# Optimization experiments

Hardware: AMD Instinct MI355X
Metric: run time of the kernel (lower is better)

Reference implementation:

```python
import jax, jax.numpy as jnp
import numpy as np

K = 32
TEMPERATURE = 1.0
EPS = 1e-12


def setup_inputs() -> dict:
    key = jax.random.key(0)
    k1, k2, k3, k4, k5 = jax.random.split(key, 5)
    N, F, B, H, C = 65536, 512, 2048, 256, 64
    X = jax.random.normal(k1, (N, F), dtype=jnp.float32)
    # non-negative PPR-like weights (dense representation of the sparse matrix)
    ppr_scores = jax.random.uniform(k2, (B, N), dtype=jnp.float32)
    s1 = 1.0 / np.sqrt(F)
    s2 = 1.0 / np.sqrt(H)
    W1 = jax.random.uniform(k3, (F, H), dtype=jnp.float32, minval=-s1, maxval=s1)
    W2 = jax.random.uniform(k4, (H, H), dtype=jnp.float32, minval=-s2, maxval=s2)
    W3 = jax.random.uniform(k5, (H, C), dtype=jnp.float32, minval=-s2, maxval=s2)
    return {"X": X, "ppr_scores": ppr_scores, "W1": W1, "W2": W2, "W3": W3}


def _mlp(X, W1, W2, W3):
    # PPRGoMLP, nlayers=3, no bias, dropout inactive at inference
    h = jnp.maximum(X @ W1, 0.0)
    h = jnp.maximum(h @ W2, 0.0)
    return h @ W3  # [N, C] logits


def _soft_k_medoid(A, x, k=K, temperature=TEMPERATURE, with_weight_correction=True):
    # A: [B, N] ppr weights, x: [N, C] embeddings
    topk_vals, topk_idx = jax.lax.top_k(A, k)          # [B, k]
    xk = x[topk_idx]                                    # [B, k, C] gathered neighbor embeddings
    # pairwise L2 distances among the top-k neighbors of each row: [B, k, k]
    d2 = jnp.sum(jnp.square(xk[:, :, None, :] - xk[:, None, :, :]), axis=-1)
    l2 = jnp.sqrt(d2 + EPS)
    # weighted sum of distances per candidate: [B, k]
    distances = jnp.einsum('bm,bcm->bc', topk_vals, l2)
    distances = jnp.where(topk_vals == 0, jnp.finfo(distances.dtype).max, distances)
    row_sum = jnp.sum(A, axis=-1, keepdims=True)        # [B, 1]
    w = jax.nn.softmax(-distances / temperature, axis=-1)
    if with_weight_correction:
        w = w * topk_vals
        w = w / jnp.sum(w, axis=-1, keepdims=True)
    return row_sum * jnp.einsum('bk,bkc->bc', w, xk)    # [B, C]


def reference(X, ppr_scores, W1, W2, W3):
    logits = _mlp(X, W1, W2, W3)
    return _soft_k_medoid(ppr_scores, logits)
```

## Files before the change

kernel.cpp:

```cpp
#include <hip/hip_runtime.h>
#include <hip/hip_bf16.h>

typedef unsigned short u16;
typedef __attribute__((ext_vector_type(8))) __bf16 bf16x8;
typedef __attribute__((ext_vector_type(4))) float f32x4;

#define AS1 __attribute__((address_space(1)))
#define AS3 __attribute__((address_space(3)))

__device__ inline void gload_lds16(const void* g, void* l) {
  __builtin_amdgcn_global_load_lds((const AS1 void*)g, (AS3 void*)l, 16, 0, 0);
}

__device__ inline u16 f2bf(float f) {
  __bf16 h = (__bf16)f;
  return __builtin_bit_cast(u16, h);
}

__device__ inline f32x4 ldnt(const f32x4* p) {
  return __builtin_nontemporal_load(p);
}

__global__ void conv_weights(const float* __restrict__ W1, const float* __restrict__ W2,
                             const float* __restrict__ W3, u16* __restrict__ w1t,
                             u16* __restrict__ w2t, u16* __restrict__ w3t) {
  int e = blockIdx.x * 256 + threadIdx.x;
  if (e < 131072) {
    int h = e >> 9, f = e & 511;
    w1t[e] = f2bf(W1[f * 256 + h]);
  } else if (e < 196608) {
    int x = e - 131072;
    int n = x >> 8, k = x & 255;
    w2t[x] = f2bf(W2[k * 256 + n]);
  } else if (e < 212992) {
    int x = e - 196608;
    int n = x >> 8, k = x & 255;
    w3t[x] = f2bf(W3[k * 64 + n]);
  }
}

__global__ __launch_bounds__(256, 2) void mlp_kernel(const float* __restrict__ X,
                                                     const u16* __restrict__ W1t,
                                                     const u16* __restrict__ W2t,
                                                     const u16* __restrict__ W3t,
                                                     float* __restrict__ lg) {
  __shared__ alignas(16) char smem[73728];
  u16* As   = (u16*)smem;
  u16* Bs   = (u16*)(smem + 8192);
  u16* h1s  = (u16*)(smem + 40960);
  u16* quad = (u16*)smem;
  u16* w3s  = (u16*)(smem + 8192);
  const int bm = blockIdx.x, t = threadIdx.x;
  const int wid = t >> 6, lane = t & 63;
  const int wr = wid >> 1, wc = wid & 1;
  const int l15 = lane & 15, lk = lane >> 4;
  const f32x4 z = {0.f, 0.f, 0.f, 0.f};

  {
    f32x4 acc[2][8];
#pragma unroll
    for (int i = 0; i < 2; ++i)
#pragma unroll
      for (int j = 0; j < 8; ++j) acc[i][j] = z;

    for (int k0 = 0; k0 < 512; k0 += 64) {
#pragma unroll
      for (int it = 0; it < 8; ++it) {
        int s = it * 256 + t;
        int n = s >> 3;
        int koff = ((s ^ (n & 7)) & 7) * 8;
        gload_lds16(W1t + (size_t)n * 512 + k0 + koff, &Bs[s * 8]);
      }
#pragma unroll
      for (int it = 0; it < 2; ++it) {
        int s = it * 256 + t;
        int row = s >> 3, c = s & 7;
        const float* src = X + (size_t)(bm * 64 + row) * 512 + k0 + c * 8;
        float4 v0 = *(const float4*)src;
        float4 v1 = *(const float4*)(src + 4);
        bf16x8 wv;
        wv[0] = (__bf16)v0.x; wv[1] = (__bf16)v0.y; wv[2] = (__bf16)v0.z; wv[3] = (__bf16)v0.w;
        wv[4] = (__bf16)v1.x; wv[5] = (__bf16)v1.y; wv[6] = (__bf16)v1.z; wv[7] = (__bf16)v1.w;
        *(bf16x8*)&As[(row * 64 + c * 8) ^ ((row & 7) << 3)] = wv;
      }
      __syncthreads();
#pragma unroll
      for (int ks = 0; ks < 2; ++ks) {
        bf16x8 af[2], bfr[8];
#pragma unroll
        for (int i = 0; i < 2; ++i) {
          int row = wr * 32 + i * 16 + l15;
          af[i] = *(const bf16x8*)&As[(row * 64 + ks * 32 + lk * 8) ^ ((row & 7) << 3)];
        }
#pragma unroll
        for (int j = 0; j < 8; ++j) {
          int n = wc * 128 + j * 16 + l15;
          bfr[j] = *(const bf16x8*)&Bs[(n * 64 + ks * 32 + lk * 8) ^ ((n & 7) << 3)];
        }
#pragma unroll
        for (int i = 0; i < 2; ++i)
#pragma unroll
          for (int j = 0; j < 8; ++j)
            acc[i][j] = __builtin_amdgcn_mfma_f32_16x16x32_bf16(af[i], bfr[j], acc[i][j], 0, 0, 0);
      }
      __syncthreads();
    }
#pragma unroll
    for (int i = 0; i < 2; ++i)
#pragma unroll
      for (int j = 0; j < 8; ++j)
#pragma unroll
        for (int r = 0; r < 4; ++r) {
          int row = wr * 32 + i * 16 + lk * 4 + r;
          int col = wc * 128 + j * 16 + l15;
          h1s[(row * 256 + col) ^ ((row & 7) << 3)] = f2bf(fmaxf(acc[i][j][r], 0.f));
        }
    __syncthreads();
  }

  f32x4 acc2[2][8];
#pragma unroll
  for (int i = 0; i < 2; ++i)
#pragma unroll
    for (int j = 0; j < 8; ++j) acc2[i][j] = z;

  for (int k0 = 0; k0 < 256; k0 += 64) {
#pragma unroll
    for (int it = 0; it < 8; ++it) {
      int s = it * 256 + t;
      int n = s >> 3;
      int koff = ((s ^ (n & 7)) & 7) * 8;
      gload_lds16(W2t + (size_t)n * 256 + k0 + koff, &Bs[s * 8]);
    }
    __syncthreads();
#pragma unroll
    for (int ks = 0; ks < 2; ++ks) {
      bf16x8 af[2], bfr[8];
#pragma unroll
      for (int i = 0; i < 2; ++i) {
        int row = wr * 32 + i * 16 + l15;
        af[i] = *(const bf16x8*)&h1s[(row * 256 + k0 + ks * 32 + lk * 8) ^ ((row & 7) << 3)];
      }
#pragma unroll
      for (int j = 0; j < 8; ++j) {
        int n = wc * 128 + j * 16 + l15;
        bfr[j] = *(const bf16x8*)&Bs[(n * 64 + ks * 32 + lk * 8) ^ ((n & 7) << 3)];
      }
#pragma unroll
      for (int i = 0; i < 2; ++i)
#pragma unroll
        for (int j = 0; j < 8; ++j)
          acc2[i][j] = __builtin_amdgcn_mfma_f32_16x16x32_bf16(af[i], bfr[j], acc2[i][j], 0, 0, 0);
    }
    __syncthreads();
  }

  f32x4 acc3[4];
#pragma unroll
  for (int j = 0; j < 4; ++j) acc3[j] = z;

#pragma unroll
  for (int kk = 0; kk < 4; ++kk) {
    if (wc == (kk >> 1)) {
#pragma unroll
      for (int i = 0; i < 2; ++i)
#pragma unroll
        for (int j4 = 0; j4 < 4; ++j4) {
          int j = (kk & 1) * 4 + j4;
#pragma unroll
          for (int r = 0; r < 4; ++r) {
            int row = wr * 32 + i * 16 + lk * 4 + r;
            int c   = j4 * 16 + l15;
            quad[(row * 64 + c) ^ ((row & 7) << 3)] = f2bf(fmaxf(acc2[i][j][r], 0.f));
          }
        }
    }
#pragma unroll
    for (int it = 0; it < 2; ++it) {
      int s = it * 256 + t;
      int col = s >> 3;
      int koff = ((s ^ (col & 7)) & 7) * 8;
      gload_lds16(W3t + (size_t)col * 256 + kk * 64 + koff, &w3s[(it * 256 + wid * 64) * 8]);
    }
    __syncthreads();
    bf16x8 af2, bfr2[4];
#pragma unroll
    for (int ks = 0; ks < 2; ++ks) {
#pragma unroll
      for (int j2 = 0; j2 < 4; ++j2) {
        int col = j2 * 16 + l15;
        bfr2[j2] = *(const bf16x8*)&w3s[(col * 64 + ks * 32 + lk * 8) ^ ((col & 7) << 3)];
      }
      {
        int row = wid * 16 + l15;
        af2 = *(const bf16x8*)&quad[(row * 64 + ks * 32 + lk * 8) ^ ((row & 7) << 3)];
      }
#pragma unroll
      for (int j2 = 0; j2 < 4; ++j2)
        acc3[j2] = __builtin_amdgcn_mfma_f32_16x16x32_bf16(af2, bfr2[j2], acc3[j2], 0, 0, 0);
    }
    __syncthreads();
  }

#pragma unroll
  for (int j2 = 0; j2 < 4; ++j2) {
    int col = j2 * 16 + l15;
#pragma unroll
    for (int r = 0; r < 4; ++r) {
      int row = wid * 16 + lk * 4 + r;
      lg[(size_t)(bm * 64 + row) * 64 + col] = acc3[j2][r];
    }
  }
}

__global__ __launch_bounds__(256) void topk_medoid(const float* __restrict__ ppr,
                                                   const float* __restrict__ lg,
                                                   float* __restrict__ out) {
  __shared__ alignas(16) char smem[13312];
  float* cvals   = (float*)smem;
  int*   cidx    = (int*)(smem + 4096);
  float* xk      = (float*)smem;
  float* l2m     = (float*)(smem + 8448);
  float* vals    = (float*)(smem + 12672);
  int*   idxs    = (int*)(smem + 12800);
  float* dist    = (float*)(smem + 12928);
  float* wgt     = (float*)(smem + 13056);
  float* partial = (float*)(smem + 13184);
  int*   cnt     = (int*)(smem + 13200);
  float* rsum    = (float*)(smem + 13204);

  const int b = blockIdx.x, t = threadIdx.x;
  const int lane = t & 63, wid = t >> 6;
  const float* row = ppr + (size_t)b * 65536;
  const f32x4* rp = (const f32x4*)row;
  const float T0 = 0.997f;

  if (t == 0) *cnt = 0;
  __syncthreads();

  float sum0 = 0.f, sum1 = 0.f, sum2 = 0.f, sum3 = 0.f;
  f32x4 cur[8], nxt[8];
#pragma unroll
  for (int i = 0; i < 8; ++i) cur[i] = ldnt(rp + i * 256 + t);

#pragma unroll 1
  for (int mb = 0; mb < 8; ++mb) {
    if (mb < 7) {
#pragma unroll
      for (int i = 0; i < 8; ++i) nxt[i] = ldnt(rp + ((mb + 1) * 8 + i) * 256 + t);
    }
#pragma unroll
    for (int i = 0; i < 8; ++i) {
      f32x4 x = cur[i];
      sum0 += x[0]; sum1 += x[1]; sum2 += x[2]; sum3 += x[3];
      float mx = fmaxf(fmaxf(x[0], x[1]), fmaxf(x[2], x[3]));
      if (mx > T0) {
        int fb = ((mb * 8 + i) * 256 + t) * 4;
#pragma unroll
        for (int j = 0; j < 4; ++j) {
          if (x[j] > T0) {
            int p = atomicAdd(cnt, 1);
            if (p < 1024) { cvals[p] = x[j]; cidx[p] = fb + j; }
          }
        }
      }
    }
    if (mb < 7) {
#pragma unroll
      for (int i = 0; i < 8; ++i) cur[i] = nxt[i];
    }
  }
  float sum = (sum0 + sum1) + (sum2 + sum3);
#pragma unroll
  for (int off = 32; off > 0; off >>= 1) sum += __shfl_down(sum, off);
  if (lane == 0) partial[wid] = sum;
  __syncthreads();

  const int ncand = *cnt;
  const int n = ncand < 1024 ? ncand : 1024;
  if (t == 0) *rsum = (partial[0] + partial[1]) + (partial[2] + partial[3]);

  if (n >= 32 && ncand <= 1024) {
    for (int p = t; p < n; p += 256) {
      float v = cvals[p];
      int id = cidx[p];
      int rank = 0;
      for (int q = 0; q < n; ++q) {
        float vq = cvals[q];
        int   iq = cidx[q];
        rank += (vq > v || (vq == v && iq < id)) ? 1 : 0;
      }
      if (rank < 32) { vals[rank] = v; idxs[rank] = id; }
    }
  } else if (wid == 0) {
    for (int r = 0; r < 32; ++r) {
      float bv = -__builtin_inff();
      int bi = 0x7fffffff;
      for (int p = lane; p < 65536; p += 64) {
        float xv = row[p];
        bool skip = false;
        for (int q = 0; q < r; ++q) skip = skip || (idxs[q] == p);
        if (!skip && (xv > bv || (xv == bv && p < bi))) { bv = xv; bi = p; }
      }
#pragma unroll
      for (int off = 32; off > 0; off >>= 1) {
        float ov = __shfl_down(bv, off);
        int   oi = __shfl_down(bi, off);
        if (ov > bv || (ov == bv && oi < bi)) { bv = ov; bi = oi; }
      }
      if (lane == 0) { vals[r] = bv; idxs[r] = bi; }
    }
  }
  __syncthreads();

  const float rs_b = *rsum;
#pragma unroll
  for (int j = 0; j < 8; ++j) {
    int s = j * 256 + t;
    int r = s >> 6, c = s & 63;
    xk[r * 65 + c] = lg[(size_t)idxs[r] * 64 + c];
  }
  __syncthreads();
#pragma unroll
  for (int j = 0; j < 4; ++j) {
    int p = j * 256 + t;
    int c = p >> 5, m = p & 31;
    float d = 0.f;
#pragma unroll
    for (int ch = 0; ch < 64; ++ch) {
      float df = xk[c * 65 + ch] - xk[m * 65 + ch];
      d += df * df;
    }
    l2m[c * 33 + m] = sqrtf(d + 1e-12f);
  }
  __syncthreads();
  if (t < 32) {
    float d = 0.f;
#pragma unroll
    for (int m = 0; m < 32; ++m) d += vals[m] * l2m[t * 33 + m];
    if (vals[t] == 0.f) d = 3.402823466e+38f;
    dist[t] = d;
  }
  __syncthreads();
  if (t == 0) {
    float mx = -3.402823466e+38f;
    for (int c = 0; c < 32; ++c) mx = fmaxf(mx, -dist[c]);
    float s = 0.f;
    for (int c = 0; c < 32; ++c) { float e = expf(-dist[c] - mx); wgt[c] = e; s += e; }
    float s2 = 0.f;
    for (int c = 0; c < 32; ++c) { wgt[c] = wgt[c] / s * vals[c]; s2 += wgt[c]; }
    float inv = 1.f / s2;
    for (int c = 0; c < 32; ++c) wgt[c] *= inv;
  }
  __syncthreads();
  if (t < 64) {
    float o = 0.f;
#pragma unroll
    for (int k = 0; k < 32; ++k) o += wgt[k] * xk[k * 65 + t];
    out[(size_t)b * 64 + t] = rs_b * o;
  }
}

extern "C" void kernel_launch(void* const* d_in, const int* in_sizes, int n_in,
                              void* d_out, int out_size, void* d_ws, size_t ws_size,
                              hipStream_t stream) {
  const float* X   = (const float*)d_in[0];
  const float* ppr = (const float*)d_in[1];
  const float* W1  = (const float*)d_in[2];
  const float* W2  = (const float*)d_in[3];
  const float* W3  = (const float*)d_in[4];
  float* out = (float*)d_out;
  char* ws = (char*)d_ws;

  u16*  w1t = (u16*)(ws + 0);
  u16*  w2t = (u16*)(ws + 262144);
  u16*  w3t = (u16*)(ws + 393216);
  float* lg = (float*)(ws + 458752);

  (void)in_sizes; (void)n_in; (void)out_size; (void)ws_size;

  conv_weights<<<832, 256, 0, stream>>>(W1, W2, W3, w1t, w2t, w3t);
  mlp_kernel<<<1024, 256, 0, stream>>>(X, w1t, w2t, w3t, lg);
  topk_medoid<<<2048, 256, 0, stream>>>(ppr, lg, out);
}
```

Measured before the change: 172.8 us.

## Double-buffer the W1/X and W2 LDS tiles with K=32 prefetch

```diff
diff --git a/kernel.cpp b/kernel.cpp
--- a/kernel.cpp
+++ b/kernel.cpp
@@ -45,8 +45,10 @@
                                                      const u16* __restrict__ W3t,
                                                      float* __restrict__ lg) {
   __shared__ alignas(16) char smem[73728];
-  u16* As   = (u16*)smem;
-  u16* Bs   = (u16*)(smem + 8192);
+  u16* As0  = (u16*)smem;
+  u16* As1  = (u16*)(smem + 4096);
+  u16* Bs0  = (u16*)(smem + 8192);
+  u16* Bs1  = (u16*)(smem + 24576);
   u16* h1s  = (u16*)(smem + 40960);
   u16* quad = (u16*)smem;
   u16* w3s  = (u16*)(smem + 8192);
@@ -63,45 +65,60 @@
 #pragma unroll
       for (int j = 0; j < 8; ++j) acc[i][j] = z;
 
-    for (int k0 = 0; k0 < 512; k0 += 64) {
-#pragma unroll
-      for (int it = 0; it < 8; ++it) {
-        int s = it * 256 + t;
-        int n = s >> 3;
-        int koff = ((s ^ (n & 7)) & 7) * 8;
-        gload_lds16(W1t + (size_t)n * 512 + k0 + koff, &Bs[s * 8]);
-      }
-#pragma unroll
-      for (int it = 0; it < 2; ++it) {
-        int s = it * 256 + t;
-        int row = s >> 3, c = s & 7;
-        const float* src = X + (size_t)(bm * 64 + row) * 512 + k0 + c * 8;
-        float4 v0 = *(const float4*)src;
-        float4 v1 = *(const float4*)(src + 4);
+#pragma unroll
+    for (int it = 0; it < 4; ++it) {
+      int s = it * 256 + t;
+      gload_lds16(W1t + (size_t)(s >> 2) * 512 + (s & 3) * 8,
+                  &Bs0[(it * 256 + wid * 64) * 8]);
+    }
+    {
+      const float* src = X + (size_t)(bm * 64 + (t >> 2)) * 512 + (t & 3) * 8;
+      float4 v0 = *(const float4*)src;
+      float4 v1 = *(const float4*)(src + 4);
+      bf16x8 wv;
+      wv[0] = (__bf16)v0.x; wv[1] = (__bf16)v0.y; wv[2] = (__bf16)v0.z; wv[3] = (__bf16)v0.w;
+      wv[4] = (__bf16)v1.x; wv[5] = (__bf16)v1.y; wv[6] = (__bf16)v1.z; wv[7] = (__bf16)v1.w;
+      *(bf16x8*)&As0[t * 8] = wv;
+    }
+    __syncthreads();
+
+#pragma unroll 1
+    for (int kt = 0; kt < 16; ++kt) {
+      u16* Ac = (kt & 1) ? As1 : As0;
+      u16* Bc = (kt & 1) ? Bs1 : Bs0;
+      u16* An = (kt & 1) ? As0 : As1;
+      u16* Bn = (kt & 1) ? Bs0 : Bs1;
+      const bool pf = kt < 15;
+      float4 v0, v1;
+      if (pf) {
+        int k0n = (kt + 1) * 32;
+#pragma unroll
+        for (int it = 0; it < 4; ++it) {
+          int s = it * 256 + t;
+          gload_lds16(W1t + (size_t)(s >> 2) * 512 + k0n + (s & 3) * 8,
+                      &Bn[(it * 256 + wid * 64) * 8]);
+        }
+        const float* src = X + (size_t)(bm * 64 + (t >> 2)) * 512 + k0n + (t & 3) * 8;
+        v0 = *(const float4*)src;
+        v1 = *(const float4*)(src + 4);
+      }
+      bf16x8 af[2], bfr[8];
+#pragma unroll
+      for (int i = 0; i < 2; ++i)
+        af[i] = *(const bf16x8*)&Ac[(wr * 32 + i * 16 + l15) * 32 + lk * 8];
+#pragma unroll
+      for (int j = 0; j < 8; ++j)
+        bfr[j] = *(const bf16x8*)&Bc[(wc * 128 + j * 16 + l15) * 32 + lk * 8];
+#pragma unroll
+      for (int i = 0; i < 2; ++i)
+#pragma unroll
+        for (int j = 0; j < 8; ++j)
+          acc[i][j] = __builtin_amdgcn_mfma_f32_16x16x32_bf16(af[i], bfr[j], acc[i][j], 0, 0, 0);
+      if (pf) {
         bf16x8 wv;
         wv[0] = (__bf16)v0.x; wv[1] = (__bf16)v0.y; wv[2] = (__bf16)v0.z; wv[3] = (__bf16)v0.w;
         wv[4] = (__bf16)v1.x; wv[5] = (__bf16)v1.y; wv[6] = (__bf16)v1.z; wv[7] = (__bf16)v1.w;
-        *(bf16x8*)&As[(row * 64 + c * 8) ^ ((row & 7) << 3)] = wv;
-      }
-      __syncthreads();
-#pragma unroll
-      for (int ks = 0; ks < 2; ++ks) {
-        bf16x8 af[2], bfr[8];
-#pragma unroll
-        for (int i = 0; i < 2; ++i) {
-          int row = wr * 32 + i * 16 + l15;
-          af[i] = *(const bf16x8*)&As[(row * 64 + ks * 32 + lk * 8) ^ ((row & 7) << 3)];
-        }
-#pragma unroll
-        for (int j = 0; j < 8; ++j) {
-          int n = wc * 128 + j * 16 + l15;
-          bfr[j] = *(const bf16x8*)&Bs[(n * 64 + ks * 32 + lk * 8) ^ ((n & 7) << 3)];
-        }
-#pragma unroll
-        for (int i = 0; i < 2; ++i)
-#pragma unroll
-          for (int j = 0; j < 8; ++j)
-            acc[i][j] = __builtin_amdgcn_mfma_f32_16x16x32_bf16(af[i], bfr[j], acc[i][j], 0, 0, 0);
+        *(bf16x8*)&An[t * 8] = wv;
       }
       __syncthreads();
     }
@@ -124,34 +141,41 @@
 #pragma unroll
     for (int j = 0; j < 8; ++j) acc2[i][j] = z;
 
-  for (int k0 = 0; k0 < 256; k0 += 64) {
-#pragma unroll
-    for (int it = 0; it < 8; ++it) {
-      int s = it * 256 + t;
-      int n = s >> 3;
-      int koff = ((s ^ (n & 7)) & 7) * 8;
-      gload_lds16(W2t + (size_t)n * 256 + k0 + koff, &Bs[s * 8]);
-    }
-    __syncthreads();
-#pragma unroll
-    for (int ks = 0; ks < 2; ++ks) {
-      bf16x8 af[2], bfr[8];
-#pragma unroll
-      for (int i = 0; i < 2; ++i) {
-        int row = wr * 32 + i * 16 + l15;
-        af[i] = *(const bf16x8*)&h1s[(row * 256 + k0 + ks * 32 + lk * 8) ^ ((row & 7) << 3)];
-      }
-#pragma unroll
-      for (int j = 0; j < 8; ++j) {
-        int n = wc * 128 + j * 16 + l15;
-        bfr[j] = *(const bf16x8*)&Bs[(n * 64 + ks * 32 + lk * 8) ^ ((n & 7) << 3)];
-      }
-#pragma unroll
-      for (int i = 0; i < 2; ++i)
-#pragma unroll
-        for (int j = 0; j < 8; ++j)
-          acc2[i][j] = __builtin_amdgcn_mfma_f32_16x16x32_bf16(af[i], bfr[j], acc2[i][j], 0, 0, 0);
-    }
+#pragma unroll
+  for (int it = 0; it < 4; ++it) {
+    int s = it * 256 + t;
+    gload_lds16(W2t + (size_t)(s >> 2) * 256 + (s & 3) * 8,
+                &Bs0[(it * 256 + wid * 64) * 8]);
+  }
+  __syncthreads();
+
+#pragma unroll 1
+  for (int kt = 0; kt < 8; ++kt) {
+    u16* Bc = (kt & 1) ? Bs1 : Bs0;
+    u16* Bn = (kt & 1) ? Bs0 : Bs1;
+    if (kt < 7) {
+      int k0n = (kt + 1) * 32;
+#pragma unroll
+      for (int it = 0; it < 4; ++it) {
+        int s = it * 256 + t;
+        gload_lds16(W2t + (size_t)(s >> 2) * 256 + k0n + (s & 3) * 8,
+                    &Bn[(it * 256 + wid * 64) * 8]);
+      }
+    }
+    bf16x8 af[2], bfr[8];
+#pragma unroll
+    for (int i = 0; i < 2; ++i) {
+      int row = wr * 32 + i * 16 + l15;
+      af[i] = *(const bf16x8*)&h1s[(row * 256 + kt * 32 + lk * 8) ^ ((row & 7) << 3)];
+    }
+#pragma unroll
+    for (int j = 0; j < 8; ++j)
+      bfr[j] = *(const bf16x8*)&Bc[(wc * 128 + j * 16 + l15) * 32 + lk * 8];
+#pragma unroll
+    for (int i = 0; i < 2; ++i)
+#pragma unroll
+      for (int j = 0; j < 8; ++j)
+        acc2[i][j] = __builtin_amdgcn_mfma_f32_16x16x32_bf16(af[i], bfr[j], acc2[i][j], 0, 0, 0);
     __syncthreads();
   }
 
```

Result: slower. 179.3 us (+3.8%).
